# Performance work log

Measured on AMD Instinct MI355X. Metric: run time of the kernel, lower is better.

Reference implementation:

```python
import jax, jax.numpy as jnp
import numpy as np

N_NODES, N_EDGES, N_GRAPHS, NUM_FEATURES, NUM_CLASSES = 100000, 1600000, 512, 128, 10
EPS = 1e-5


def gat_conv(x, W, a_src, a_dst, b, src, dst, heads, out_ch):
    # PyG GATConv: h = xW -> [N,H,C]; per-node scores; leaky_relu; segment softmax over dst; scatter-add
    N = x.shape[0]
    h = (x @ W).reshape(N, heads, out_ch)
    s_src = jnp.einsum('nhc,hc->nh', h, a_src)
    s_dst = jnp.einsum('nhc,hc->nh', h, a_dst)
    score = jax.nn.leaky_relu(s_src[src] + s_dst[dst], 0.2)          # [E,H]
    m = jax.ops.segment_max(score, dst, num_segments=N)              # stable softmax per dst node
    e = jnp.exp(score - m[dst])
    denom = jax.ops.segment_sum(e, dst, num_segments=N)
    alpha = e / denom[dst]                                            # self-loops guarantee denom>0
    out = jax.ops.segment_sum(alpha[:, :, None] * h[src], dst, num_segments=N)
    return out.reshape(N, heads * out_ch) + b


def batch_norm(x, g, b):
    mu = x.mean(0)
    var = x.var(0)  # biased, as torch BN uses for normalization
    return g * (x - mu) * jax.lax.rsqrt(var + EPS) + b


def setup_inputs() -> dict:
    key = jax.random.key(0)
    ks = jax.random.split(key, 32)
    r = lambda i, shape: jax.random.normal(ks[i], shape, dtype=jnp.float32) * 0.1
    inp = {
        'x': jax.random.normal(ks[0], (N_NODES, NUM_FEATURES), dtype=jnp.float32),
        'edge_index': jax.random.randint(ks[1], (2, N_EDGES), 0, N_NODES, dtype=jnp.int64),
        'batch': jnp.sort(jax.random.randint(ks[2], (N_NODES,), 0, N_GRAPHS, dtype=jnp.int64)),
        # conv1: 128 -> 8 ch x 8 heads
        'W1': r(3, (NUM_FEATURES, 64)), 'a1s': r(4, (8, 8)), 'a1d': r(5, (8, 8)), 'b1': r(6, (64,)),
        'g1': jnp.ones(64), 'be1': jnp.zeros(64),
        'lW1': r(7, (64, 8)), 'lb1': r(8, (8,)), 'gl1': jnp.ones(8), 'bel1': jnp.zeros(8),
        # conv2: 8 -> 16 ch x 4 heads
        'W2': r(9, (8, 64)), 'a2s': r(10, (4, 16)), 'a2d': r(11, (4, 16)), 'b2': r(12, (64,)),
        'g2': jnp.ones(64), 'be2': jnp.zeros(64),
        'lW2': r(13, (64, 16)), 'lb2': r(14, (16,)), 'gl2': jnp.ones(16), 'bel2': jnp.zeros(16),
        # conv3: 16 -> 24 ch x 4 heads
        'W3': r(15, (16, 96)), 'a3s': r(16, (4, 24)), 'a3d': r(17, (4, 24)), 'b3': r(18, (96,)),
        'g3': jnp.ones(96), 'be3': jnp.zeros(96),
        'oW': r(19, (96, NUM_CLASSES)), 'ob': r(20, (NUM_CLASSES,)),
    }
    return inp


def reference(x, edge_index, batch, W1, a1s, a1d, b1, g1, be1, lW1, lb1, gl1, bel1,
              W2, a2s, a2d, b2, g2, be2, lW2, lb2, gl2, bel2,
              W3, a3s, a3d, b3, g3, be3, oW, ob):
    N = x.shape[0]
    loops = jnp.arange(N, dtype=edge_index.dtype)
    src = jnp.concatenate([edge_index[0], loops])  # PyG add_self_loops default
    dst = jnp.concatenate([edge_index[1], loops])

    h = gat_conv(x, W1, a1s, a1d, b1, src, dst, 8, 8)
    h = jax.nn.relu(batch_norm(h, g1, be1))
    h = jax.nn.relu(batch_norm(h @ lW1 + lb1, gl1, bel1))

    h = gat_conv(h, W2, a2s, a2d, b2, src, dst, 4, 16)
    h = jax.nn.relu(batch_norm(h, g2, be2))
    h = jax.nn.relu(batch_norm(h @ lW2 + lb2, gl2, bel2))

    h = gat_conv(h, W3, a3s, a3d, b3, src, dst, 4, 24)
    h = jax.nn.relu(batch_norm(h, g3, be3))

    sums = jax.ops.segment_sum(h, batch, num_segments=N_GRAPHS)
    cnts = jax.ops.segment_sum(jnp.ones((N,), h.dtype), batch, num_segments=N_GRAPHS)
    pooled = sums / jnp.maximum(cnts, 1.0)[:, None]
    return pooled @ oW + ob
```

## Files before the change

### kernel.cpp

```cpp
#include <hip/hip_runtime.h>
#include <hip/hip_fp16.h>
#include <math.h>

#define NN 100000
#define NE 1600000
#define ET (NE + NN)
#define NG 512
#define STATS_BLOCKS 240
#define SCAN_B 1024
#define SCAN_NB ((NN + SCAN_B - 1) / SCAN_B)
#define PSLOTS (ET + 7 * NN + 16)

#define BSH 9
#define NB  ((NN + 511) / 512)
#define BCAP 12288
#define CHUNK 4096


__global__ __launch_bounds__(256) void part_pass1(const int* __restrict__ ei,
                                                  int* __restrict__ bcur,
                                                  unsigned* __restrict__ pairs) {
    __shared__ unsigned pck[CHUNK];
    __shared__ unsigned ordv[CHUNK];
    __shared__ unsigned char bkt[CHUNK];
    __shared__ unsigned char obkt[CHUNK];
    __shared__ int hist[NB + 1];
    __shared__ int lofs[NB + 1];
    __shared__ int cur[NB + 1];
    __shared__ int gpos[NB];
    __shared__ int lh[256];

    int t = threadIdx.x;
    int base = blockIdx.x * CHUNK;
    for (int i = t; i <= NB; i += 256) hist[i] = 0;
    __syncthreads();
    for (int i = t; i < CHUNK; i += 256) {
        int e = base + i;
        int b;
        unsigned p = 0;
        if (e < ET) {
            int s, d;
            if (e < NE) { s = ei[e]; d = ei[NE + e]; }
            else        { s = d = e - NE; }
            b = d >> BSH;
            p = ((unsigned)s << BSH) | (unsigned)(d & 511);
        } else b = NB;
        bkt[i] = (unsigned char)b;
        pck[i] = p;
        atomicAdd(&hist[b], 1);
    }
    __syncthreads();
    int v = (t <= NB) ? hist[t] : 0;
    lh[t] = v;
    __syncthreads();
    for (int off = 1; off < 256; off <<= 1) {
        int x = (t >= off) ? lh[t - off] : 0;
        __syncthreads();
        lh[t] += x;
        __syncthreads();
    }
    if (t <= NB) { lofs[t] = lh[t] - v; cur[t] = lh[t] - v; }
    __syncthreads();
    if (t < NB) {
        int h = hist[t];
        gpos[t] = (h > 0) ? atomicAdd(&bcur[t], h) : 0;
    }
    __syncthreads();
    for (int i = t; i < CHUNK; i += 256) {
        int b = bkt[i];
        int pos = atomicAdd(&cur[b], 1);
        ordv[pos] = pck[i];
        obkt[pos] = (unsigned char)b;
    }
    __syncthreads();
    int nvalid = lofs[NB];
    for (int i = t; i < nvalid; i += 256) {
        int b = obkt[i];
        int dst = gpos[b] + (i - lofs[b]);
        if (dst < BCAP) pairs[(size_t)b * BCAP + dst] = ordv[i];
    }
}


__global__ __launch_bounds__(256) void bucket_counts(const unsigned* __restrict__ pairs,
                                                     const int* __restrict__ bcur,
                                                     int* __restrict__ counts) {
    __shared__ int lhist[512];
    int b = blockIdx.x;
    int t = threadIdx.x;
    for (int i = t; i < 512; i += 256) lhist[i] = 0;
    __syncthreads();
    int cnt = min(bcur[b], BCAP);
    const unsigned* seg = pairs + (size_t)b * BCAP;
    for (int i = t; i < cnt; i += 256)
        atomicAdd(&lhist[seg[i] & 511], 1);
    __syncthreads();
    int nbase = b << BSH;
    for (int i = t; i < 512; i += 256) {
        int n = nbase + i;
        if (n < NN) counts[n] = lhist[i];
    }
}


__global__ __launch_bounds__(256) void bucket_scatter(const unsigned* __restrict__ pairs,
                                                      const int* __restrict__ bcur,
                                                      const int* __restrict__ offsets,
                                                      int* __restrict__ srcs) {
    __shared__ int cur[512];
    int b = blockIdx.x;
    int t = threadIdx.x;
    int nbase = b << BSH;
    for (int i = t; i < 512; i += 256) {
        int n = nbase + i;
        cur[i] = (n < NN) ? offsets[n] : 0;
    }
    __syncthreads();
    int cnt = min(bcur[b], BCAP);
    const unsigned* seg = pairs + (size_t)b * BCAP;
    for (int i = t; i < cnt; i += 256) {
        unsigned p = seg[i];
        int pos = atomicAdd(&cur[p & 511], 1);
        srcs[pos] = (int)(p >> BSH);
    }
}


__global__ void graph_bounds(const int* __restrict__ batch, int* __restrict__ goff) {
    int g = blockIdx.x * blockDim.x + threadIdx.x;
    if (g > NG) return;
    int lo = 0, hi = NN;
    while (lo < hi) {
        int mid = (lo + hi) >> 1;
        if (batch[mid] < g) lo = mid + 1; else hi = mid;
    }
    goff[g] = lo;
}


__global__ void scan_reduce(const int* __restrict__ in, int* __restrict__ bsum) {
    __shared__ int lds[256];
    int b = blockIdx.x, t = threadIdx.x;
    int s = 0;
    for (int i = t; i < SCAN_B; i += 256) {
        int idx = b * SCAN_B + i;
        if (idx < NN) s += (in[idx] + 7) & ~7;
    }
    lds[t] = s;
    __syncthreads();
    for (int off = 128; off > 0; off >>= 1) {
        if (t < off) lds[t] += lds[t + off];
        __syncthreads();
    }
    if (t == 0) bsum[b] = lds[0];
}

__global__ void scan_bsums(const int* __restrict__ bsum, int nb, int* __restrict__ boff,
                           int* __restrict__ total_loc) {
    __shared__ int lds[128];
    int t = threadIdx.x;
    int v = (t < nb) ? bsum[t] : 0;
    lds[t] = v;
    __syncthreads();
    for (int off = 1; off < 128; off <<= 1) {
        int x = (t >= off) ? lds[t - off] : 0;
        __syncthreads();
        lds[t] += x;
        __syncthreads();
    }
    if (t < nb) boff[t] = lds[t] - v;
    if (t == nb - 1) {
        boff[nb] = lds[t];
        if (total_loc) *total_loc = lds[t];
    }
}

__global__ void scan_final(const int* __restrict__ in, const int* __restrict__ boff,
                           int* __restrict__ out) {
    __shared__ int lds[SCAN_B];
    int b = blockIdx.x, t = threadIdx.x;
    int idx = b * SCAN_B + t;
    int v = (idx < NN) ? ((in[idx] + 7) & ~7) : 0;
    lds[t] = v;
    __syncthreads();
    for (int off = 1; off < SCAN_B; off <<= 1) {
        int x = (t >= off) ? lds[t - off] : 0;
        __syncthreads();
        lds[t] += x;
        __syncthreads();
    }
    if (idx < NN) out[idx] = boff[b] + lds[t] - v;
}


__global__ __launch_bounds__(256) void gemm1(const float* __restrict__ X,
                                             const float* __restrict__ W,
                                             const float* __restrict__ a_s,
                                             const float* __restrict__ a_d,
                                             __half* __restrict__ Hh,
                                             float* __restrict__ SS,
                                             float* __restrict__ SD) {
    __shared__ float wl[128 * 64];
    __shared__ float xl[32 * 132];
    int t = threadIdx.x;
    int n0 = blockIdx.x * 32;
    for (int i = t * 4; i < 128 * 64; i += 1024)
        *(float4*)&wl[i] = *(const float4*)&W[i];
    for (int i = t * 4; i < 32 * 128; i += 1024) {
        int r = i >> 7, c = i & 127;
        int n = n0 + r;
        float4 v = (n < NN) ? *(const float4*)&X[(size_t)n * 128 + c] : make_float4(0, 0, 0, 0);
        *(float4*)&xl[r * 132 + c] = v;
    }
    __syncthreads();
    int cg = (t & 15) * 4;
    int ng = (t >> 4) * 2;
    float acc[2][4] = {};
    for (int k = 0; k < 128; ++k) {
        float4 w4 = *(float4*)&wl[k * 64 + cg];
        #pragma unroll
        for (int j = 0; j < 2; ++j) {
            float xv = xl[(ng + j) * 132 + k];
            acc[j][0] += xv * w4.x; acc[j][1] += xv * w4.y;
            acc[j][2] += xv * w4.z; acc[j][3] += xv * w4.w;
        }
    }
    int hd = cg >> 3;
    int half = cg & 7;
    #pragma unroll
    for (int j = 0; j < 2; ++j) {
        int n = n0 + ng + j;
        float p1 = 0.f, p2 = 0.f;
        #pragma unroll
        for (int k = 0; k < 4; ++k) {
            p1 += acc[j][k] * a_s[hd * 8 + half + k];
            p2 += acc[j][k] * a_d[hd * 8 + half + k];
        }
        float f1 = p1 + __shfl_xor(p1, 1, 64);
        float f2 = p2 + __shfl_xor(p2, 1, 64);
        if (n < NN) {
            __half2 q0 = __floats2half2_rn(acc[j][0], acc[j][1]);
            __half2 q1 = __floats2half2_rn(acc[j][2], acc[j][3]);
            *(__half2*)&Hh[(size_t)n * 64 + cg] = q0;
            *(__half2*)&Hh[(size_t)n * 64 + cg + 2] = q1;
            if (half == 0) {
                SS[(unsigned)n * 8 + hd] = f1;
                SD[(unsigned)n * 8 + hd] = f2;
            }
        }
    }
}


template <int HEADS, int C, int PL, int GRP>
__global__ __launch_bounds__(256) void gat_kernel(const __half* __restrict__ Hh,
                                                  const float* __restrict__ SS,
                                                  const float* __restrict__ SD,
                                                  const int* __restrict__ offsets,
                                                  const int* __restrict__ counts,
                                                  const int* __restrict__ srcs,
                                                  const float* __restrict__ bias,
                                                  __half* __restrict__ GO) {
    constexpr int CH = HEADS * C;
    constexpr int LG = (GRP == 16) ? 4 : 3;
    int wid = blockIdx.x * (blockDim.x >> 6) + (threadIdx.x >> 6);
    int lane = threadIdx.x & 63;
    if (wid >= NN) return;
    int ch0 = lane * PL;
    bool active = ch0 < CH;
    int ch0l = active ? ch0 : 0;
    int head = active ? (ch0 / C) : 0;
    int headGRP = head * GRP;
    int beg = offsets[wid], end = offsets[wid + 1];
    int deg = counts[wid];
    int sEdge = lane & (GRP - 1);
    int sHead = (lane >> LG) & (HEADS - 1);
    float sdvS = SD[(unsigned)wid * HEADS + sHead];
    float s = 0.f, a0 = 0.f, a1 = 0.f;
    for (int e = beg; e < end; e += GRP) {
        int myIdx = e + sEdge;
        int mySrc = srcs[myIdx];
        float sc = SS[(unsigned)mySrc * HEADS + sHead] + sdvS;
        sc = fmaxf(sc, 0.f) + 0.2f * fminf(sc, 0.f);
        float myW = (myIdx - beg) < deg ? __expf(sc) : 0.f;
        int sv[GRP];
        float wv[GRP];
        #pragma unroll
        for (int i = 0; i < GRP; ++i) {
            sv[i] = __shfl(mySrc, headGRP + i, 64);
            wv[i] = __shfl(myW, headGRP + i, 64);
        }
        if (PL == 1) {
            float hv[GRP];
            #pragma unroll
            for (int i = 0; i < GRP; ++i)
                hv[i] = __half2float(Hh[(unsigned)(sv[i] * CH) + ch0l]);
            float pw[GRP / 2], pa[GRP / 2];
            #pragma unroll
            for (int i = 0; i < GRP / 2; ++i) {
                pw[i] = wv[2 * i] + wv[2 * i + 1];
                pa[i] = wv[2 * i] * hv[2 * i] + wv[2 * i + 1] * hv[2 * i + 1];
            }
            #pragma unroll
            for (int st = GRP / 4; st >= 1; st >>= 1) {
                #pragma unroll
                for (int i = 0; i < st; ++i) { pw[i] += pw[i + st]; pa[i] += pa[i + st]; }
            }
            s += pw[0];
            a0 += pa[0];
        } else {
            float hv0[GRP], hv1[GRP];
            #pragma unroll
            for (int i = 0; i < GRP; ++i) {
                __half2 hp = *(const __half2*)&Hh[(unsigned)(sv[i] * CH) + ch0l];
                hv0[i] = __low2float(hp); hv1[i] = __high2float(hp);
            }
            float pw[GRP / 2], pa[GRP / 2], pb[GRP / 2];
            #pragma unroll
            for (int i = 0; i < GRP / 2; ++i) {
                pw[i] = wv[2 * i] + wv[2 * i + 1];
                pa[i] = wv[2 * i] * hv0[2 * i] + wv[2 * i + 1] * hv0[2 * i + 1];
                pb[i] = wv[2 * i] * hv1[2 * i] + wv[2 * i + 1] * hv1[2 * i + 1];
            }
            #pragma unroll
            for (int st = GRP / 4; st >= 1; st >>= 1) {
                #pragma unroll
                for (int i = 0; i < st; ++i) { pw[i] += pw[i + st]; pa[i] += pa[i + st]; pb[i] += pb[i + st]; }
            }
            s += pw[0];
            a0 += pa[0];
            a1 += pb[0];
        }
    }
    if (active) {
        float inv = 1.f / s;
        if (PL == 2) {
            *(__half2*)&GO[(unsigned)(wid * CH) + ch0] =
                __floats2half2_rn(a0 * inv + bias[ch0], a1 * inv + bias[ch0 + 1]);
        } else {
            GO[(unsigned)(wid * CH) + ch0] = __float2half(a0 * inv + bias[ch0]);
        }
    }
}


__global__ void stats_kernel(const float* __restrict__ X, int Nn, int C,
                             float* __restrict__ partial) {
    int t = threadIdx.x;
    int c = t % C;
    int grp = t / C;
    int G_ = blockDim.x / C;
    float s = 0.f, q = 0.f;
    for (int n = blockIdx.x * G_ + grp; n < Nn; n += gridDim.x * G_) {
        float v = X[(size_t)n * C + c];
        s += v; q += v * v;
    }
    extern __shared__ float lds[];
    lds[t] = s; lds[blockDim.x + t] = q;
    __syncthreads();
    for (int off = blockDim.x >> 1; off >= C; off >>= 1) {
        if (t < off) {
            lds[t] += lds[t + off];
            lds[blockDim.x + t] += lds[blockDim.x + t + off];
        }
        __syncthreads();
    }
    if (t < C) {
        partial[(size_t)blockIdx.x * 2 * C + t] = lds[t];
        partial[(size_t)blockIdx.x * 2 * C + C + t] = lds[blockDim.x + t];
    }
}

__global__ void stats_h_kernel(const __half* __restrict__ X, int Nn, int C,
                               float* __restrict__ partial) {
    int t = threadIdx.x;
    int C2 = C >> 1;
    int cp = t % C2;
    int grp = t / C2;
    int G_ = blockDim.x / C2;
    float s0 = 0.f, q0 = 0.f, s1 = 0.f, q1 = 0.f;
    for (int n = blockIdx.x * G_ + grp; n < Nn; n += gridDim.x * G_) {
        float2 v = __half22float2(*(const __half2*)&X[(size_t)n * C + cp * 2]);
        s0 += v.x; q0 += v.x * v.x;
        s1 += v.y; q1 += v.y * v.y;
    }
    extern __shared__ float lds[];
    float* L0 = lds;
    float* L1 = lds + blockDim.x;
    float* L2 = lds + 2 * blockDim.x;
    float* L3 = lds + 3 * blockDim.x;
    L0[t] = s0; L1[t] = s1; L2[t] = q0; L3[t] = q1;
    __syncthreads();
    for (int off = blockDim.x >> 1; off >= C2; off >>= 1) {
        if (t < off) {
            L0[t] += L0[t + off];
            L1[t] += L1[t + off];
            L2[t] += L2[t + off];
            L3[t] += L3[t + off];
        }
        __syncthreads();
    }
    if (t < C2) {
        partial[(size_t)blockIdx.x * 2 * C + 2 * t]     = L0[t];
        partial[(size_t)blockIdx.x * 2 * C + 2 * t + 1] = L1[t];
        partial[(size_t)blockIdx.x * 2 * C + C + 2 * t]     = L2[t];
        partial[(size_t)blockIdx.x * 2 * C + C + 2 * t + 1] = L3[t];
    }
}

__global__ void bn_finalize(const float* __restrict__ partial, int nb, int C, float invN,
                            const float* __restrict__ g, const float* __restrict__ be,
                            float* __restrict__ scale, float* __restrict__ shift) {
    extern __shared__ float red[];
    int t = threadIdx.x;
    int c = t % C;
    int grp = t / C;
    int G_ = blockDim.x / C;
    float s = 0.f, q = 0.f;
    for (int b = grp; b < nb; b += G_) {
        s += partial[(size_t)b * 2 * C + c];
        q += partial[(size_t)b * 2 * C + C + c];
    }
    red[t] = s; red[blockDim.x + t] = q;
    __syncthreads();
    for (int off = blockDim.x >> 1; off >= C; off >>= 1) {
        if (t < off) {
            red[t] += red[t + off];
            red[blockDim.x + t] += red[blockDim.x + t + off];
        }
        __syncthreads();
    }
    if (t < C) {
        float mean = red[t] * invN;
        float var = fmaxf(red[blockDim.x + t] * invN - mean * mean, 0.f);
        float rs = rsqrtf(var + 1e-5f);
        float sc = g[t] * rs;
        scale[t] = sc;
        shift[t] = be[t] - mean * sc;
    }
}


template <int KOUT>
__global__ __launch_bounds__(256) void bnrelu_linear(const __half* __restrict__ X,
                                                     const float* __restrict__ scale,
                                                     const float* __restrict__ shift,
                                                     const float* __restrict__ Lw,
                                                     const float* __restrict__ lb,
                                                     float* __restrict__ U) {
    __shared__ float tl[64 * 65];
    int t = threadIdx.x;
    int n0 = blockIdx.x * 64;
    for (int i = t * 4; i < 64 * 64; i += 1024) {
        int r = i >> 6, cc = i & 63;
        int n = n0 + r;
        float vv[4] = {0.f, 0.f, 0.f, 0.f};
        if (n < NN) {
            float2 v0 = __half22float2(*(const __half2*)&X[(size_t)n * 64 + cc]);
            float2 v1 = __half22float2(*(const __half2*)&X[(size_t)n * 64 + cc + 2]);
            vv[0] = v0.x; vv[1] = v0.y; vv[2] = v1.x; vv[3] = v1.y;
        }
        #pragma unroll
        for (int j = 0; j < 4; ++j)
            tl[r * 65 + cc + j] = fmaxf(vv[j] * scale[cc + j] + shift[cc + j], 0.f);
    }
    __syncthreads();
    int nl = t & 63;
    int kg = (t >> 6) * (KOUT / 4);
    float acc[KOUT / 4] = {};
    for (int l = 0; l < 64; ++l) {
        float v = tl[nl * 65 + l];
        #pragma unroll
        for (int j = 0; j < KOUT / 4; ++j) acc[j] += v * Lw[l * KOUT + kg + j];
    }
    int n = n0 + nl;
    if (n < NN)
        #pragma unroll
        for (int j = 0; j < KOUT / 4; ++j)
            U[(size_t)n * KOUT + kg + j] = acc[j] + lb[kg + j];
}


template <int CIN, int COUT, int H, int C>
__global__ __launch_bounds__(256) void bnrelu_gemm(const float* __restrict__ U,
                                                   const float* __restrict__ scale,
                                                   const float* __restrict__ shift,
                                                   const float* __restrict__ W,
                                                   const float* __restrict__ a_s,
                                                   const float* __restrict__ a_d,
                                                   __half* __restrict__ Hh,
                                                   float* __restrict__ SS,
                                                   float* __restrict__ SD) {
    static_assert(COUT / 4 == C && H == 4, "thread-per-head mapping");
    int t = threadIdx.x;
    int nl = t >> 2;
    int q = t & 3;
    int n = blockIdx.x * 64 + nl;
    if (n >= NN) return;
    constexpr int CPT = COUT / 4;
    float v[CIN];
    #pragma unroll
    for (int c = 0; c < CIN; ++c)
        v[c] = fmaxf(U[(size_t)n * CIN + c] * scale[c] + shift[c], 0.f);
    float acc[CPT] = {};
    #pragma unroll
    for (int c = 0; c < CIN; ++c) {
        #pragma unroll
        for (int j = 0; j < CPT; ++j) acc[j] += v[c] * W[c * COUT + q * CPT + j];
    }
    float s1 = 0.f, s2 = 0.f;
    #pragma unroll
    for (int j = 0; j < CPT; ++j) {
        s1 += acc[j] * a_s[q * C + j];
        s2 += acc[j] * a_d[q * C + j];
    }
    SS[(unsigned)n * H + q] = s1;
    SD[(unsigned)n * H + q] = s2;
    #pragma unroll
    for (int j = 0; j < CPT; j += 2)
        *(__half2*)&Hh[(size_t)n * COUT + q * CPT + j] = __floats2half2_rn(acc[j], acc[j + 1]);
}


__global__ __launch_bounds__(128) void pool_kernel(const __half* __restrict__ GO,
                                                   const float* __restrict__ scale,
                                                   const float* __restrict__ shift,
                                                   const int* __restrict__ goff,
                                                   float* __restrict__ pooled) {
    __shared__ float red[8][16][2];
    int g = blockIdx.x;
    int lp = threadIdx.x & 15;
    int row = threadIdx.x >> 4;
    int ch = blockIdx.y * 32 + lp * 2;
    int beg = goff[g], end = goff[g + 1];
    float sc0 = scale[ch], sh0 = shift[ch];
    float sc1 = scale[ch + 1], sh1 = shift[ch + 1];
    float s0 = 0.f, s1 = 0.f;
    for (int n = beg + row; n < end; n += 8) {
        float2 v = __half22float2(*(const __half2*)&GO[(size_t)n * 96 + ch]);
        s0 += fmaxf(v.x * sc0 + sh0, 0.f);
        s1 += fmaxf(v.y * sc1 + sh1, 0.f);
    }
    red[row][lp][0] = s0;
    red[row][lp][1] = s1;
    __syncthreads();
    if (row == 0) {
        #pragma unroll
        for (int r = 1; r < 8; ++r) { s0 += red[r][lp][0]; s1 += red[r][lp][1]; }
        float cnt = fmaxf((float)(end - beg), 1.f);
        pooled[g * 96 + ch] = s0 / cnt;
        pooled[g * 96 + ch + 1] = s1 / cnt;
    }
}

__global__ void final_gemm(const float* __restrict__ pooled, const float* __restrict__ oW,
                           const float* __restrict__ ob, float* __restrict__ out) {
    int idx = blockIdx.x * blockDim.x + threadIdx.x;
    if (idx >= NG * 10) return;
    int g = idx / 10, k = idx % 10;
    float s = ob[k];
    for (int c = 0; c < 96; ++c) s += pooled[g * 96 + c] * oW[c * 10 + k];
    out[idx] = s;
}


extern "C" void kernel_launch(void* const* d_in, const int* in_sizes, int n_in,
                              void* d_out, int out_size, void* d_ws, size_t ws_size,
                              hipStream_t stream) {
    const float* x   = (const float*)d_in[0];
    const int*   ei  = (const int*)d_in[1];
    const int*   bat = (const int*)d_in[2];
    const float *W1 = (const float*)d_in[3], *a1s = (const float*)d_in[4],
                *a1d = (const float*)d_in[5], *b1 = (const float*)d_in[6],
                *g1 = (const float*)d_in[7], *be1 = (const float*)d_in[8],
                *lW1 = (const float*)d_in[9], *lb1 = (const float*)d_in[10],
                *gl1 = (const float*)d_in[11], *bel1 = (const float*)d_in[12],
                *W2 = (const float*)d_in[13], *a2s = (const float*)d_in[14],
                *a2d = (const float*)d_in[15], *b2 = (const float*)d_in[16],
                *g2 = (const float*)d_in[17], *be2 = (const float*)d_in[18],
                *lW2 = (const float*)d_in[19], *lb2 = (const float*)d_in[20],
                *gl2 = (const float*)d_in[21], *bel2 = (const float*)d_in[22],
                *W3 = (const float*)d_in[23], *a3s = (const float*)d_in[24],
                *a3d = (const float*)d_in[25], *b3 = (const float*)d_in[26],
                *g3 = (const float*)d_in[27], *be3 = (const float*)d_in[28],
                *oW = (const float*)d_in[29], *ob = (const float*)d_in[30];
    float* out = (float*)d_out;

    int* iw      = (int*)d_ws;
    int* bcur    = iw;
    int* counts  = bcur + NB;
    int* offsets = counts + NN;
    int* goff    = offsets + NN + 1;
    int* bsum    = goff + NG + 1;
    int* boff    = bsum + SCAN_NB;
    int* srcs    = boff + SCAN_NB + 1;
    float* fw      = (float*)(srcs + PSLOTS);
    __half* GOh    = (__half*)fw;
    float* Ub      = fw + (size_t)NN * 96;
    float* SSb     = Ub + (size_t)NN * 16;
    float* SDb     = SSb + (size_t)NN * 8;
    float* partial = SDb + (size_t)NN * 8;
    float* scaleA  = partial + STATS_BLOCKS * 192;
    float* shiftA  = scaleA + 96;
    float* scaleB  = shiftA + 96;
    float* shiftB  = scaleB + 16;
    float* pooled  = shiftB + 16;
    __half* Hh     = (__half*)(pooled + NG * 96);
    unsigned* pairs = (unsigned*)GOh;

    const float invN = 1.0f / (float)NN;

    hipMemsetAsync(bcur, 0, NB * sizeof(int), stream);
    hipMemsetAsync(srcs, 0, (size_t)PSLOTS * sizeof(int), stream);
    part_pass1<<<(ET + CHUNK - 1) / CHUNK, 256, 0, stream>>>(ei, bcur, pairs);
    graph_bounds<<<3, 256, 0, stream>>>(bat, goff);
    bucket_counts<<<NB, 256, 0, stream>>>(pairs, bcur, counts);
    scan_reduce<<<SCAN_NB, 256, 0, stream>>>(counts, bsum);
    scan_bsums<<<1, 128, 0, stream>>>(bsum, SCAN_NB, boff, &offsets[NN]);
    scan_final<<<SCAN_NB, SCAN_B, 0, stream>>>(counts, boff, offsets);
    bucket_scatter<<<NB, 256, 0, stream>>>(pairs, bcur, offsets, srcs);

    gemm1<<<(NN + 31) / 32, 256, 0, stream>>>(x, W1, a1s, a1d, Hh, SSb, SDb);
    gat_kernel<8, 8, 1, 8><<<(NN + 3) / 4, 256, 0, stream>>>(Hh, SSb, SDb, offsets, counts, srcs, b1, GOh);
    stats_h_kernel<<<STATS_BLOCKS, 256, 4 * 256 * sizeof(float), stream>>>(GOh, NN, 64, partial);
    bn_finalize<<<1, 512, 2 * 512 * sizeof(float), stream>>>(partial, STATS_BLOCKS, 64, invN, g1, be1, scaleA, shiftA);
    bnrelu_linear<8><<<(NN + 63) / 64, 256, 0, stream>>>(GOh, scaleA, shiftA, lW1, lb1, Ub);
    stats_kernel<<<STATS_BLOCKS, 256, 2 * 256 * sizeof(float), stream>>>(Ub, NN, 8, partial);
    bn_finalize<<<1, 512, 2 * 512 * sizeof(float), stream>>>(partial, STATS_BLOCKS, 8, invN, gl1, bel1, scaleB, shiftB);

    bnrelu_gemm<8, 64, 4, 16><<<(NN + 63) / 64, 256, 0, stream>>>(Ub, scaleB, shiftB, W2, a2s, a2d, Hh, SSb, SDb);
    gat_kernel<4, 16, 1, 16><<<(NN + 3) / 4, 256, 0, stream>>>(Hh, SSb, SDb, offsets, counts, srcs, b2, GOh);
    stats_h_kernel<<<STATS_BLOCKS, 256, 4 * 256 * sizeof(float), stream>>>(GOh, NN, 64, partial);
    bn_finalize<<<1, 512, 2 * 512 * sizeof(float), stream>>>(partial, STATS_BLOCKS, 64, invN, g2, be2, scaleA, shiftA);
    bnrelu_linear<16><<<(NN + 63) / 64, 256, 0, stream>>>(GOh, scaleA, shiftA, lW2, lb2, Ub);
    stats_kernel<<<STATS_BLOCKS, 256, 2 * 256 * sizeof(float), stream>>>(Ub, NN, 16, partial);
    bn_finalize<<<1, 512, 2 * 512 * sizeof(float), stream>>>(partial, STATS_BLOCKS, 16, invN, gl2, bel2, scaleB, shiftB);

    bnrelu_gemm<16, 96, 4, 24><<<(NN + 63) / 64, 256, 0, stream>>>(Ub, scaleB, shiftB, W3, a3s, a3d, Hh, SSb, SDb);
    gat_kernel<4, 24, 2, 8><<<(NN + 3) / 4, 256, 0, stream>>>(Hh, SSb, SDb, offsets, counts, srcs, b3, GOh);
    stats_h_kernel<<<STATS_BLOCKS, 192, 4 * 192 * sizeof(float), stream>>>(GOh, NN, 96, partial);
    bn_finalize<<<1, 768, 2 * 768 * sizeof(float), stream>>>(partial, STATS_BLOCKS, 96, invN, g3, be3, scaleA, shiftA);

    pool_kernel<<<dim3(NG, 3), 128, 0, stream>>>(GOh, scaleA, shiftA, goff, pooled);
    final_gemm<<<(NG * 10 + 255) / 256, 256, 0, stream>>>(pooled, oW, ob, out);
}
```

Baseline: 559.0 us.

## Fuse scan, BN finalize, and pooling head kernels to cut launch count

Folds the per-bucket padded-count reduction into bucket_counts and replaces the three-kernel scan with a bucket-aligned scan. A single zero-fill memset of the whole srcs buffer is dropped; padding slots are now zeroed inside bucket_scatter. BN finalize is merged into the stats kernels using a last-block-done atomic counter, and pooling is fused with the output GEMM. This removes about a dozen small launches and one large memset, at the cost of threadfence/atomic ordering and a serial final reduction in one block.

After: 650.9 us. +16.4%, slower.

```diff
diff --git a/kernel.cpp b/kernel.cpp
--- a/kernel.cpp
+++ b/kernel.cpp
@@ -7,8 +7,6 @@
 #define ET (NE + NN)
 #define NG 512
 #define STATS_BLOCKS 240
-#define SCAN_B 1024
-#define SCAN_NB ((NN + SCAN_B - 1) / SCAN_B)
 #define PSLOTS (ET + 7 * NN + 16)
 
 #define BSH 9
@@ -84,8 +82,10 @@
 
 __global__ __launch_bounds__(256) void bucket_counts(const unsigned* __restrict__ pairs,
                                                      const int* __restrict__ bcur,
-                                                     int* __restrict__ counts) {
+                                                     int* __restrict__ counts,
+                                                     int* __restrict__ bsum) {
     __shared__ int lhist[512];
+    __shared__ int rs[256];
     int b = blockIdx.x;
     int t = threadIdx.x;
     for (int i = t; i < 512; i += 256) lhist[i] = 0;
@@ -96,10 +96,61 @@
         atomicAdd(&lhist[seg[i] & 511], 1);
     __syncthreads();
     int nbase = b << BSH;
+    int ps = 0;
     for (int i = t; i < 512; i += 256) {
         int n = nbase + i;
-        if (n < NN) counts[n] = lhist[i];
-    }
+        int h = lhist[i];
+        if (n < NN) {
+            counts[n] = h;
+            ps += (h + 7) & ~7;
+        }
+    }
+    rs[t] = ps;
+    __syncthreads();
+    for (int off = 128; off > 0; off >>= 1) {
+        if (t < off) rs[t] += rs[t + off];
+        __syncthreads();
+    }
+    if (t == 0) bsum[b] = rs[0];
+}
+
+
+__global__ void scan_buckets(const int* __restrict__ bsum, int* __restrict__ boff,
+                             int* __restrict__ total_loc, int* __restrict__ srcs) {
+    __shared__ int lds[256];
+    int t = threadIdx.x;
+    int v = (t < NB) ? bsum[t] : 0;
+    lds[t] = v;
+    __syncthreads();
+    for (int off = 1; off < 256; off <<= 1) {
+        int x = (t >= off) ? lds[t - off] : 0;
+        __syncthreads();
+        lds[t] += x;
+        __syncthreads();
+    }
+    if (t < NB) boff[t] = lds[t] - v;
+    int total = lds[255];
+    if (t == NB - 1) { boff[NB] = total; *total_loc = total; }
+    if (t < 16) srcs[total + t] = 0;
+}
+
+
+__global__ __launch_bounds__(512) void scan_final_bucket(const int* __restrict__ counts,
+                                                         const int* __restrict__ boff,
+                                                         int* __restrict__ offsets) {
+    __shared__ int lds[512];
+    int b = blockIdx.x, t = threadIdx.x;
+    int n = (b << BSH) + t;
+    int v = (n < NN) ? ((counts[n] + 7) & ~7) : 0;
+    lds[t] = v;
+    __syncthreads();
+    for (int off = 1; off < 512; off <<= 1) {
+        int x = (t >= off) ? lds[t - off] : 0;
+        __syncthreads();
+        lds[t] += x;
+        __syncthreads();
+    }
+    if (n < NN) offsets[n] = boff[b] + lds[t] - v;
 }
 
 
@@ -122,6 +173,16 @@
         unsigned p = seg[i];
         int pos = atomicAdd(&cur[p & 511], 1);
         srcs[pos] = (int)(p >> BSH);
+    }
+    __syncthreads();
+    for (int i = t; i < 512; i += 256) {
+        int n = nbase + i;
+        if (n < NN) {
+            int o = offsets[n];
+            int fin = cur[i];
+            int padEnd = o + ((fin - o + 7) & ~7);
+            for (int p = fin; p < padEnd; ++p) srcs[p] = 0;
+        }
     }
 }
 
@@ -135,61 +196,6 @@
         if (batch[mid] < g) lo = mid + 1; else hi = mid;
     }
     goff[g] = lo;
-}
-
-
-__global__ void scan_reduce(const int* __restrict__ in, int* __restrict__ bsum) {
-    __shared__ int lds[256];
-    int b = blockIdx.x, t = threadIdx.x;
-    int s = 0;
-    for (int i = t; i < SCAN_B; i += 256) {
-        int idx = b * SCAN_B + i;
-        if (idx < NN) s += (in[idx] + 7) & ~7;
-    }
-    lds[t] = s;
-    __syncthreads();
-    for (int off = 128; off > 0; off >>= 1) {
-        if (t < off) lds[t] += lds[t + off];
-        __syncthreads();
-    }
-    if (t == 0) bsum[b] = lds[0];
-}
-
-__global__ void scan_bsums(const int* __restrict__ bsum, int nb, int* __restrict__ boff,
-                           int* __restrict__ total_loc) {
-    __shared__ int lds[128];
-    int t = threadIdx.x;
-    int v = (t < nb) ? bsum[t] : 0;
-    lds[t] = v;
-    __syncthreads();
-    for (int off = 1; off < 128; off <<= 1) {
-        int x = (t >= off) ? lds[t - off] : 0;
-        __syncthreads();
-        lds[t] += x;
-        __syncthreads();
-    }
-    if (t < nb) boff[t] = lds[t] - v;
-    if (t == nb - 1) {
-        boff[nb] = lds[t];
-        if (total_loc) *total_loc = lds[t];
-    }
-}
-
-__global__ void scan_final(const int* __restrict__ in, const int* __restrict__ boff,
-                           int* __restrict__ out) {
-    __shared__ int lds[SCAN_B];
-    int b = blockIdx.x, t = threadIdx.x;
-    int idx = b * SCAN_B + t;
-    int v = (idx < NN) ? ((in[idx] + 7) & ~7) : 0;
-    lds[t] = v;
-    __syncthreads();
-    for (int off = 1; off < SCAN_B; off <<= 1) {
-        int x = (t >= off) ? lds[t - off] : 0;
-        __syncthreads();
-        lds[t] += x;
-        __syncthreads();
-    }
-    if (idx < NN) out[idx] = boff[b] + lds[t] - v;
 }
 
 
@@ -344,8 +350,11 @@
 }
 
 
-__global__ void stats_kernel(const float* __restrict__ X, int Nn, int C,
-                             float* __restrict__ partial) {
+__global__ void stats_fused(const float* __restrict__ X, int Nn, int C, float invN,
+                            const float* __restrict__ g, const float* __restrict__ be,
+                            float* __restrict__ partial, int* __restrict__ done,
+                            float* __restrict__ scale, float* __restrict__ shift) {
+    extern __shared__ float lds[];
     int t = threadIdx.x;
     int c = t % C;
     int grp = t / C;
@@ -355,7 +364,6 @@
         float v = X[(size_t)n * C + c];
         s += v; q += v * v;
     }
-    extern __shared__ float lds[];
     lds[t] = s; lds[blockDim.x + t] = q;
     __syncthreads();
     for (int off = blockDim.x >> 1; off >= C; off >>= 1) {
@@ -369,10 +377,44 @@
         partial[(size_t)blockIdx.x * 2 * C + t] = lds[t];
         partial[(size_t)blockIdx.x * 2 * C + C + t] = lds[blockDim.x + t];
     }
-}
-
-__global__ void stats_h_kernel(const __half* __restrict__ X, int Nn, int C,
-                               float* __restrict__ partial) {
+    __threadfence();
+    __shared__ int isLast;
+    __syncthreads();
+    if (t == 0) isLast = (atomicAdd(done, 1) == (int)gridDim.x - 1);
+    __syncthreads();
+    if (!isLast) return;
+    __threadfence();
+    float fs = 0.f, fq = 0.f;
+    for (int b = grp; b < (int)gridDim.x; b += G_) {
+        fs += partial[(size_t)b * 2 * C + c];
+        fq += partial[(size_t)b * 2 * C + C + c];
+    }
+    __syncthreads();
+    lds[t] = fs; lds[blockDim.x + t] = fq;
+    __syncthreads();
+    for (int off = blockDim.x >> 1; off >= C; off >>= 1) {
+        if (t < off) {
+            lds[t] += lds[t + off];
+            lds[blockDim.x + t] += lds[blockDim.x + t + off];
+        }
+        __syncthreads();
+    }
+    if (t < C) {
+        float mean = lds[t] * invN;
+        float var = fmaxf(lds[blockDim.x + t] * invN - mean * mean, 0.f);
+        float rs = rsqrtf(var + 1e-5f);
+        float sc = g[t] * rs;
+        scale[t] = sc;
+        shift[t] = be[t] - mean * sc;
+    }
+}
+
+
+__global__ void stats_h_fused(const __half* __restrict__ X, int Nn, int C, float invN,
+                              const float* __restrict__ g, const float* __restrict__ be,
+                              float* __restrict__ partial, int* __restrict__ done,
+                              float* __restrict__ scale, float* __restrict__ shift) {
+    extern __shared__ float lds[];
     int t = threadIdx.x;
     int C2 = C >> 1;
     int cp = t % C2;
@@ -384,7 +426,6 @@
         s0 += v.x; q0 += v.x * v.x;
         s1 += v.y; q1 += v.y * v.y;
     }
-    extern __shared__ float lds[];
     float* L0 = lds;
     float* L1 = lds + blockDim.x;
     float* L2 = lds + 2 * blockDim.x;
@@ -406,33 +447,34 @@
         partial[(size_t)blockIdx.x * 2 * C + C + 2 * t]     = L2[t];
         partial[(size_t)blockIdx.x * 2 * C + C + 2 * t + 1] = L3[t];
     }
-}
-
-__global__ void bn_finalize(const float* __restrict__ partial, int nb, int C, float invN,
-                            const float* __restrict__ g, const float* __restrict__ be,
-                            float* __restrict__ scale, float* __restrict__ shift) {
-    extern __shared__ float red[];
-    int t = threadIdx.x;
+    __threadfence();
+    __shared__ int isLast;
+    __syncthreads();
+    if (t == 0) isLast = (atomicAdd(done, 1) == (int)gridDim.x - 1);
+    __syncthreads();
+    if (!isLast) return;
+    __threadfence();
     int c = t % C;
-    int grp = t / C;
-    int G_ = blockDim.x / C;
-    float s = 0.f, q = 0.f;
-    for (int b = grp; b < nb; b += G_) {
-        s += partial[(size_t)b * 2 * C + c];
-        q += partial[(size_t)b * 2 * C + C + c];
-    }
-    red[t] = s; red[blockDim.x + t] = q;
+    int fg = t / C;
+    int FG = blockDim.x / C;
+    float fs = 0.f, fq = 0.f;
+    for (int b = fg; b < (int)gridDim.x; b += FG) {
+        fs += partial[(size_t)b * 2 * C + c];
+        fq += partial[(size_t)b * 2 * C + C + c];
+    }
+    __syncthreads();
+    lds[t] = fs; lds[blockDim.x + t] = fq;
     __syncthreads();
     for (int off = blockDim.x >> 1; off >= C; off >>= 1) {
         if (t < off) {
-            red[t] += red[t + off];
-            red[blockDim.x + t] += red[blockDim.x + t + off];
+            lds[t] += lds[t + off];
+            lds[blockDim.x + t] += lds[blockDim.x + t + off];
         }
         __syncthreads();
     }
     if (t < C) {
-        float mean = red[t] * invN;
-        float var = fmaxf(red[blockDim.x + t] * invN - mean * mean, 0.f);
+        float mean = lds[t] * invN;
+        float var = fmaxf(lds[blockDim.x + t] * invN - mean * mean, 0.f);
         float rs = rsqrtf(var + 1e-5f);
         float sc = g[t] * rs;
         scale[t] = sc;
@@ -522,45 +564,46 @@
 }
 
 
-__global__ __launch_bounds__(128) void pool_kernel(const __half* __restrict__ GO,
-                                                   const float* __restrict__ scale,
-                                                   const float* __restrict__ shift,
-                                                   const int* __restrict__ goff,
-                                                   float* __restrict__ pooled) {
+__global__ __launch_bounds__(128) void pool_head(const __half* __restrict__ GO,
+                                                 const float* __restrict__ scale,
+                                                 const float* __restrict__ shift,
+                                                 const int* __restrict__ goff,
+                                                 const float* __restrict__ oW,
+                                                 const float* __restrict__ ob,
+                                                 float* __restrict__ out) {
     __shared__ float red[8][16][2];
+    __shared__ float pl[96];
     int g = blockIdx.x;
     int lp = threadIdx.x & 15;
     int row = threadIdx.x >> 4;
-    int ch = blockIdx.y * 32 + lp * 2;
     int beg = goff[g], end = goff[g + 1];
-    float sc0 = scale[ch], sh0 = shift[ch];
-    float sc1 = scale[ch + 1], sh1 = shift[ch + 1];
-    float s0 = 0.f, s1 = 0.f;
-    for (int n = beg + row; n < end; n += 8) {
-        float2 v = __half22float2(*(const __half2*)&GO[(size_t)n * 96 + ch]);
-        s0 += fmaxf(v.x * sc0 + sh0, 0.f);
-        s1 += fmaxf(v.y * sc1 + sh1, 0.f);
-    }
-    red[row][lp][0] = s0;
-    red[row][lp][1] = s1;
-    __syncthreads();
-    if (row == 0) {
-        #pragma unroll
-        for (int r = 1; r < 8; ++r) { s0 += red[r][lp][0]; s1 += red[r][lp][1]; }
-        float cnt = fmaxf((float)(end - beg), 1.f);
-        pooled[g * 96 + ch] = s0 / cnt;
-        pooled[g * 96 + ch + 1] = s1 / cnt;
-    }
-}
-
-__global__ void final_gemm(const float* __restrict__ pooled, const float* __restrict__ oW,
-                           const float* __restrict__ ob, float* __restrict__ out) {
-    int idx = blockIdx.x * blockDim.x + threadIdx.x;
-    if (idx >= NG * 10) return;
-    int g = idx / 10, k = idx % 10;
-    float s = ob[k];
-    for (int c = 0; c < 96; ++c) s += pooled[g * 96 + c] * oW[c * 10 + k];
-    out[idx] = s;
+    for (int cg = 0; cg < 3; ++cg) {
+        int ch = cg * 32 + lp * 2;
+        float sc0 = scale[ch], sh0 = shift[ch];
+        float sc1 = scale[ch + 1], sh1 = shift[ch + 1];
+        float s0 = 0.f, s1 = 0.f;
+        for (int n = beg + row; n < end; n += 8) {
+            float2 v = __half22float2(*(const __half2*)&GO[(size_t)n * 96 + ch]);
+            s0 += fmaxf(v.x * sc0 + sh0, 0.f);
+            s1 += fmaxf(v.y * sc1 + sh1, 0.f);
+        }
+        red[row][lp][0] = s0;
+        red[row][lp][1] = s1;
+        __syncthreads();
+        if (row == 0) {
+            #pragma unroll
+            for (int r = 1; r < 8; ++r) { s0 += red[r][lp][0]; s1 += red[r][lp][1]; }
+            float cnt = fmaxf((float)(end - beg), 1.f);
+            pl[ch] = s0 / cnt;
+            pl[ch + 1] = s1 / cnt;
+        }
+        __syncthreads();
+    }
+    if (threadIdx.x < 10) {
+        float s = ob[threadIdx.x];
+        for (int c = 0; c < 96; ++c) s += pl[c] * oW[c * 10 + threadIdx.x];
+        out[g * 10 + threadIdx.x] = s;
+    }
 }
 
 
@@ -588,12 +631,13 @@
 
     int* iw      = (int*)d_ws;
     int* bcur    = iw;
-    int* counts  = bcur + NB;
+    int* done    = bcur + NB;
+    int* counts  = done + 8;
     int* offsets = counts + NN;
     int* goff    = offsets + NN + 1;
     int* bsum    = goff + NG + 1;
-    int* boff    = bsum + SCAN_NB;
-    int* srcs    = boff + SCAN_NB + 1;
+    int* boff    = bsum + NB;
+    int* srcs    = boff + NB + 1;
     float* fw      = (float*)(srcs + PSLOTS);
     __half* GOh    = (__half*)fw;
     float* Ub      = fw + (size_t)NN * 96;
@@ -604,43 +648,34 @@
     float* shiftA  = scaleA + 96;
     float* scaleB  = shiftA + 96;
     float* shiftB  = scaleB + 16;
-    float* pooled  = shiftB + 16;
-    __half* Hh     = (__half*)(pooled + NG * 96);
+    __half* Hh     = (__half*)(shiftB + 16);
     unsigned* pairs = (unsigned*)GOh;
 
     const float invN = 1.0f / (float)NN;
 
-    hipMemsetAsync(bcur, 0, NB * sizeof(int), stream);
-    hipMemsetAsync(srcs, 0, (size_t)PSLOTS * sizeof(int), stream);
+    hipMemsetAsync(bcur, 0, (NB + 8) * sizeof(int), stream);
     part_pass1<<<(ET + CHUNK - 1) / CHUNK, 256, 0, stream>>>(ei, bcur, pairs);
     graph_bounds<<<3, 256, 0, stream>>>(bat, goff);
-    bucket_counts<<<NB, 256, 0, stream>>>(pairs, bcur, counts);
-    scan_reduce<<<SCAN_NB, 256, 0, stream>>>(counts, bsum);
-    scan_bsums<<<1, 128, 0, stream>>>(bsum, SCAN_NB, boff, &offsets[NN]);
-    scan_final<<<SCAN_NB, SCAN_B, 0, stream>>>(counts, boff, offsets);
+    bucket_counts<<<NB, 256, 0, stream>>>(pairs, bcur, counts, bsum);
+    scan_buckets<<<1, 256, 0, stream>>>(bsum, boff, &offsets[NN], srcs);
+    scan_final_bucket<<<NB, 512, 0, stream>>>(counts, boff, offsets);
     bucket_scatter<<<NB, 256, 0, stream>>>(pairs, bcur, offsets, srcs);
 
     gemm1<<<(NN + 31) / 32, 256, 0, stream>>>(x, W1, a1s, a1d, Hh, SSb, SDb);
     gat_kernel<8, 8, 1, 8><<<(NN + 3) / 4, 256, 0, stream>>>(Hh, SSb, SDb, offsets, counts, srcs, b1, GOh);
-    stats_h_kernel<<<STATS_BLOCKS, 256, 4 * 256 * sizeof(float), stream>>>(GOh, NN, 64, partial);
-    bn_finalize<<<1, 512, 2 * 512 * sizeof(float), stream>>>(partial, STATS_BLOCKS, 64, invN, g1, be1, scaleA, shiftA);
+    stats_h_fused<<<STATS_BLOCKS, 256, 4 * 256 * sizeof(float), stream>>>(GOh, NN, 64, invN, g1, be1, partial, done + 0, scaleA, shiftA);
     bnrelu_linear<8><<<(NN + 63) / 64, 256, 0, stream>>>(GOh, scaleA, shiftA, lW1, lb1, Ub);
-    stats_kernel<<<STATS_BLOCKS, 256, 2 * 256 * sizeof(float), stream>>>(Ub, NN, 8, partial);
-    bn_finalize<<<1, 512, 2 * 512 * sizeof(float), stream>>>(partial, STATS_BLOCKS, 8, invN, gl1, bel1, scaleB, shiftB);
+    stats_fused<<<STATS_BLOCKS, 256, 4 * 256 * sizeof(float), stream>>>(Ub, NN, 8, invN, gl1, bel1, partial, done + 1, scaleB, shiftB);
 
     bnrelu_gemm<8, 64, 4, 16><<<(NN + 63) / 64, 256, 0, stream>>>(Ub, scaleB, shiftB, W2, a2s, a2d, Hh, SSb, SDb);
     gat_kernel<4, 16, 1, 16><<<(NN + 3) / 4, 256, 0, stream>>>(Hh, SSb, SDb, offsets, counts, srcs, b2, GOh);
-    stats_h_kernel<<<STATS_BLOCKS, 256, 4 * 256 * sizeof(float), stream>>>(GOh, NN, 64, partial);
-    bn_finalize<<<1, 512, 2 * 512 * sizeof(float), stream>>>(partial, STATS_BLOCKS, 64, invN, g2, be2, scaleA, shiftA);
+    stats_h_fused<<<STATS_BLOCKS, 256, 4 * 256 * sizeof(float), stream>>>(GOh, NN, 64, invN, g2, be2, partial, done + 2, scaleA, shiftA);
     bnrelu_linear<16><<<(NN + 63) / 64, 256, 0, stream>>>(GOh, scaleA, shiftA, lW2, lb2, Ub);
-    stats_kernel<<<STATS_BLOCKS, 256, 2 * 256 * sizeof(float), stream>>>(Ub, NN, 16, partial);
-    bn_finalize<<<1, 512, 2 * 512 * sizeof(float), stream>>>(partial, STATS_BLOCKS, 16, invN, gl2, bel2, scaleB, shiftB);
+    stats_fused<<<STATS_BLOCKS, 256, 4 * 256 * sizeof(float), stream>>>(Ub, NN, 16, invN, gl2, bel2, partial, done + 3, scaleB, shiftB);
 
     bnrelu_gemm<16, 96, 4, 24><<<(NN + 63) / 64, 256, 0, stream>>>(Ub, scaleB, shiftB, W3, a3s, a3d, Hh, SSb, SDb);
     gat_kernel<4, 24, 2, 8><<<(NN + 3) / 4, 256, 0, stream>>>(Hh, SSb, SDb, offsets, counts, srcs, b3, GOh);
-    stats_h_kernel<<<STATS_BLOCKS, 192, 4 * 192 * sizeof(float), stream>>>(GOh, NN, 96, partial);
-    bn_finalize<<<1, 768, 2 * 768 * sizeof(float), stream>>>(partial, STATS_BLOCKS, 96, invN, g3, be3, scaleA, shiftA);
-
-    pool_kernel<<<dim3(NG, 3), 128, 0, stream>>>(GOh, scaleA, shiftA, goff, pooled);
-    final_gemm<<<(NG * 10 + 255) / 256, 256, 0, stream>>>(pooled, oW, ob, out);
-}
+    stats_h_fused<<<STATS_BLOCKS, 192, 4 * 192 * sizeof(float), stream>>>(GOh, NN, 96, invN, g3, be3, partial, done + 4, scaleA, shiftA);
+
+    pool_head<<<NG, 128, 0, stream>>>(GOh, scaleA, shiftA, goff, oW, ob, out);
+}
```
